# Kernel tuning notes

Measured on AMD Instinct MI355X. Metric: run time of the kernel, lower is better.

Reference implementation:

```python
import jax, jax.numpy as jnp
import numpy as np

N_NODES = 50000
D_IN = 128
D_OUT = 128
N_EDGES = 800000


def setup_inputs() -> dict:
    key = jax.random.key(0)
    k1, k2, k3, k4 = jax.random.split(key, 4)
    x = jax.random.normal(k1, (N_NODES, D_IN), dtype=jnp.float32)
    # nn.Linear(input_size, output_size, bias=False): weight is [out, in], y = x @ W.T.
    # We store W1 as [in, out] so y = x @ W1 (same math, transposed storage).
    W1 = jax.random.normal(k2, (D_IN, D_OUT), dtype=jnp.float32) * (1.0 / np.sqrt(D_IN))
    row = jax.random.randint(k3, (N_EDGES,), 0, N_NODES, dtype=jnp.int64)
    col = jax.random.randint(k4, (N_EDGES,), 0, N_NODES, dtype=jnp.int64)
    edge_index = jnp.stack([row, col], axis=0)  # [2, E]
    return {"x": x, "W1": W1, "edge_index": edge_index}


def reference(x, W1, edge_index):
    # Linear transform: [N, D_in] @ [D_in, D_out] -> [N, D_out]
    norm_m = x @ W1
    adj_row = edge_index[0]  # source nodes (gather)
    adj_col = edge_index[1]  # destination nodes (scatter)
    gathered = norm_m[adj_row]  # [E, D_out]
    pooled = jax.ops.segment_max(gathered, adj_col, num_segments=x.shape[0])
    # torch_scatter fills segments with no incoming edges with 0 (not -inf)
    deg = jax.ops.segment_sum(jnp.ones_like(adj_col, dtype=jnp.int32), adj_col,
                              num_segments=x.shape[0])
    pooled = jnp.where((deg > 0)[:, None], pooled, jnp.zeros_like(pooled))
    return jnp.concatenate((x, pooled), axis=1)  # [N, D_in + D_out]
```

## Files before the change

kernel.cpp:

```cpp
#include <hip/hip_runtime.h>


#define N_DIN 128
#define CAP 64
#define CURSTRIDE 16

typedef __attribute__((ext_vector_type(8))) short bf16x8;
typedef __attribute__((ext_vector_type(4))) float f32x4;

__device__ __forceinline__ short f32_bf16(float f) {
    unsigned u = __float_as_uint(f);
    return (short)((u + 0x7fffu + ((u >> 16) & 1u)) >> 16);
}

__global__ __launch_bounds__(256) void wconv(const float* __restrict__ W,
                                             short* __restrict__ Wt) {
    int i = blockIdx.x * 256 + threadIdx.x;
    int k = i >> 5, n0 = (i & 31) * 4;
    float4 v = *(const float4*)(W + k * 128 + n0);
    Wt[(n0 + 0) * 128 + k] = f32_bf16(v.x);
    Wt[(n0 + 1) * 128 + k] = f32_bf16(v.y);
    Wt[(n0 + 2) * 128 + k] = f32_bf16(v.z);
    Wt[(n0 + 3) * 128 + k] = f32_bf16(v.w);
}

__global__ __launch_bounds__(256) void scatter_direct(const int* __restrict__ row,
                                                      const int* __restrict__ col,
                                                      int* __restrict__ cur,
                                                      int* __restrict__ csrc, int E) {
    int e = blockIdx.x * 256 + threadIdx.x;
    if (e >= E) return;
    int dst = col[e];
    int pos = atomicAdd(&cur[dst * CURSTRIDE], 1);
    if (pos < CAP) csrc[dst * CAP + pos] = row[e];
}

__global__ __launch_bounds__(256) void gemm_mfma(const float* __restrict__ X,
                                                 const short* __restrict__ Wt,
                                                 short* __restrict__ Yb,
                                                 float* __restrict__ out, int N) {
    __shared__ short c_lds[4][32][128];
    const int tid = threadIdx.x;
    const int w = tid >> 6, l = tid & 63;
    const int lr = l & 15, lg = l >> 4;
    const int R0 = blockIdx.x * 128 + w * 32;

    bf16x8 af[2][4];
#pragma unroll
    for (int rt = 0; rt < 2; ++rt) {
        int gr = R0 + rt * 16 + lr;
        int grc = gr < N ? gr : N - 1;
#pragma unroll
        for (int t = 0; t < 4; ++t) {
            int kc = t * 32 + lg * 8;
            float4 v0 = *(const float4*)(X + (size_t)grc * 128 + kc);
            float4 v1 = *(const float4*)(X + (size_t)grc * 128 + kc + 4);
            if (gr < N) {
                *(float4*)(out + (size_t)gr * 256 + kc)     = v0;
                *(float4*)(out + (size_t)gr * 256 + kc + 4) = v1;
            }
            bf16x8 a;
            a[0] = f32_bf16(v0.x); a[1] = f32_bf16(v0.y);
            a[2] = f32_bf16(v0.z); a[3] = f32_bf16(v0.w);
            a[4] = f32_bf16(v1.x); a[5] = f32_bf16(v1.y);
            a[6] = f32_bf16(v1.z); a[7] = f32_bf16(v1.w);
            af[rt][t] = a;
        }
    }
#pragma unroll
    for (int ct = 0; ct < 8; ++ct) {
        f32x4 c0 = {0.f, 0.f, 0.f, 0.f}, c1 = {0.f, 0.f, 0.f, 0.f};
        const short* bp = Wt + (ct * 16 + lr) * 128;
#pragma unroll
        for (int t = 0; t < 4; ++t) {
            bf16x8 b = *(const bf16x8*)(bp + t * 32 + lg * 8);
            c0 = __builtin_amdgcn_mfma_f32_16x16x32_bf16(af[0][t], b, c0, 0, 0, 0);
            c1 = __builtin_amdgcn_mfma_f32_16x16x32_bf16(af[1][t], b, c1, 0, 0, 0);
        }
#pragma unroll
        for (int i = 0; i < 4; ++i) {
            c_lds[w][lg * 4 + i][ct * 16 + lr]      = f32_bf16(c0[i]);
            c_lds[w][16 + lg * 4 + i][ct * 16 + lr] = f32_bf16(c1[i]);
        }
    }
#pragma unroll
    for (int it = 0; it < 8; ++it) {
        int cid = it * 64 + l;
        int r2 = cid >> 4, c2 = cid & 15;
        int gr = R0 + r2;
        if (gr < N) {
            bf16x8 vv = *(const bf16x8*)(&c_lds[w][r2][c2 * 8]);
            *(bf16x8*)(Yb + (size_t)gr * 128 + c2 * 8) = vv;
        }
    }
}

__global__ __launch_bounds__(256) void pool_bf16(const unsigned* __restrict__ nmb,
                                                 const int* __restrict__ cur,
                                                 const int* __restrict__ csrc,
                                                 float* __restrict__ out, int N) {
    int node = blockIdx.x * 4 + (threadIdx.x >> 6);
    if (node >= N) return;
    int lane = threadIdx.x & 63;
    int deg = cur[node * CURSTRIDE];
    if (deg > CAP) deg = CAP;
    const int* lst = csrc + node * CAP;
    float2 acc = make_float2(-INFINITY, -INFINITY);
    int j = 0;
    for (; j + 4 <= deg; j += 4) {
        int s0 = lst[j], s1 = lst[j + 1], s2 = lst[j + 2], s3 = lst[j + 3];
        unsigned v0 = nmb[s0 * 64 + lane];
        unsigned v1 = nmb[s1 * 64 + lane];
        unsigned v2 = nmb[s2 * 64 + lane];
        unsigned v3 = nmb[s3 * 64 + lane];
        acc.x = fmaxf(acc.x, fmaxf(fmaxf(__uint_as_float(v0 << 16), __uint_as_float(v1 << 16)),
                                   fmaxf(__uint_as_float(v2 << 16), __uint_as_float(v3 << 16))));
        acc.y = fmaxf(acc.y, fmaxf(fmaxf(__uint_as_float(v0 & 0xffff0000u), __uint_as_float(v1 & 0xffff0000u)),
                                   fmaxf(__uint_as_float(v2 & 0xffff0000u), __uint_as_float(v3 & 0xffff0000u))));
    }
    for (; j < deg; ++j) {
        unsigned v0 = nmb[lst[j] * 64 + lane];
        acc.x = fmaxf(acc.x, __uint_as_float(v0 << 16));
        acc.y = fmaxf(acc.y, __uint_as_float(v0 & 0xffff0000u));
    }
    if (deg == 0) acc = make_float2(0.f, 0.f);
    *(float2*)(out + (size_t)node * 256 + N_DIN + lane * 2) = acc;
}

extern "C" void kernel_launch(void* const* d_in, const int* in_sizes, int n_in,
                              void* d_out, int out_size, void* d_ws, size_t ws_size,
                              hipStream_t stream) {
    const float* x  = (const float*)d_in[0];
    const float* W1 = (const float*)d_in[1];
    const int* ei   = (const int*)d_in[2];
    const int N = in_sizes[0] / N_DIN;
    const int E = in_sizes[2] / 2;
    const int* row = ei;
    const int* col = ei + E;
    float* out = (float*)d_out;

    short* norm_mb = (short*)d_ws;
    short* Wt = norm_mb + (size_t)N * N_DIN;
    int* cur  = (int*)(Wt + 128 * 128);
    int* csrc = cur + (size_t)N * CURSTRIDE;

    hipMemsetAsync(cur, 0, (size_t)N * CURSTRIDE * sizeof(int), stream);
    wconv<<<16, 256, 0, stream>>>(W1, Wt);
    scatter_direct<<<(E + 255) / 256, 256, 0, stream>>>(row, col, cur, csrc, E);
    gemm_mfma<<<(N + 127) / 128, 256, 0, stream>>>(x, Wt, norm_mb, out, N);
    pool_bf16<<<(N + 3) / 4, 256, 0, stream>>>((const unsigned*)norm_mb, cur, csrc, out, N);
}
```

Measured before the change: 187.2 us.

## Fuse edge scatter into GEMM launch and compact CSR index storage

Merges the edge-bucketing scatter kernel into the MFMA GEMM kernel as extra blocks so both run concurrently in one launch. Removes the 16-int padding on per-node counters, shrinking the memset and the counter footprint. Stores neighbor source indices as 16-bit values, halving index traffic in the scatter and pool phases. This relies on the node count fitting in 16 bits. The unpadded counters may add some atomic contention within cache lines.

```diff
diff --git a/kernel.cpp b/kernel.cpp
--- a/kernel.cpp
+++ b/kernel.cpp
@@ -3,7 +3,6 @@
 
 #define N_DIN 128
 #define CAP 64
-#define CURSTRIDE 16
 
 typedef __attribute__((ext_vector_type(8))) short bf16x8;
 typedef __attribute__((ext_vector_type(4))) float f32x4;
@@ -24,26 +23,26 @@
     Wt[(n0 + 3) * 128 + k] = f32_bf16(v.w);
 }
 
-__global__ __launch_bounds__(256) void scatter_direct(const int* __restrict__ row,
-                                                      const int* __restrict__ col,
-                                                      int* __restrict__ cur,
-                                                      int* __restrict__ csrc, int E) {
-    int e = blockIdx.x * 256 + threadIdx.x;
-    if (e >= E) return;
-    int dst = col[e];
-    int pos = atomicAdd(&cur[dst * CURSTRIDE], 1);
-    if (pos < CAP) csrc[dst * CAP + pos] = row[e];
-}
-
-__global__ __launch_bounds__(256) void gemm_mfma(const float* __restrict__ X,
-                                                 const short* __restrict__ Wt,
-                                                 short* __restrict__ Yb,
-                                                 float* __restrict__ out, int N) {
+__global__ __launch_bounds__(256) void fused_gemm_scatter(
+        const float* __restrict__ X, const short* __restrict__ Wt,
+        short* __restrict__ Yb, float* __restrict__ out, int N, int gblocks,
+        const int* __restrict__ row, const int* __restrict__ col,
+        int* __restrict__ cur, unsigned short* __restrict__ csrc, int E) {
+    if ((int)blockIdx.x >= gblocks) {
+        int e = ((int)blockIdx.x - gblocks) * 256 + (int)threadIdx.x;
+        if (e < E) {
+            int dst = col[e];
+            int pos = atomicAdd(&cur[dst], 1);
+            if (pos < CAP)
+                csrc[dst * CAP + pos] = (unsigned short)row[e];
+        }
+        return;
+    }
     __shared__ short c_lds[4][32][128];
     const int tid = threadIdx.x;
     const int w = tid >> 6, l = tid & 63;
     const int lr = l & 15, lg = l >> 4;
-    const int R0 = blockIdx.x * 128 + w * 32;
+    const int R0 = (int)blockIdx.x * 128 + w * 32;
 
     bf16x8 af[2][4];
 #pragma unroll
@@ -97,14 +96,14 @@
 
 __global__ __launch_bounds__(256) void pool_bf16(const unsigned* __restrict__ nmb,
                                                  const int* __restrict__ cur,
-                                                 const int* __restrict__ csrc,
+                                                 const unsigned short* __restrict__ csrc,
                                                  float* __restrict__ out, int N) {
     int node = blockIdx.x * 4 + (threadIdx.x >> 6);
     if (node >= N) return;
     int lane = threadIdx.x & 63;
-    int deg = cur[node * CURSTRIDE];
+    int deg = cur[node];
     if (deg > CAP) deg = CAP;
-    const int* lst = csrc + node * CAP;
+    const unsigned short* lst = csrc + node * CAP;
     float2 acc = make_float2(-INFINITY, -INFINITY);
     int j = 0;
     for (; j + 4 <= deg; j += 4) {
@@ -142,11 +141,14 @@
     short* norm_mb = (short*)d_ws;
     short* Wt = norm_mb + (size_t)N * N_DIN;
     int* cur  = (int*)(Wt + 128 * 128);
-    int* csrc = cur + (size_t)N * CURSTRIDE;
+    unsigned short* csrc = (unsigned short*)(cur + N);
 
-    hipMemsetAsync(cur, 0, (size_t)N * CURSTRIDE * sizeof(int), stream);
+    const int gblocks = (N + 127) / 128;
+    const int sblocks = (E + 255) / 256;
+
+    hipMemsetAsync(cur, 0, (size_t)N * sizeof(int), stream);
     wconv<<<16, 256, 0, stream>>>(W1, Wt);
-    scatter_direct<<<(E + 255) / 256, 256, 0, stream>>>(row, col, cur, csrc, E);
-    gemm_mfma<<<(N + 127) / 128, 256, 0, stream>>>(x, Wt, norm_mb, out, N);
+    fused_gemm_scatter<<<gblocks + sblocks, 256, 0, stream>>>(
+        x, Wt, norm_mb, out, N, gblocks, row, col, cur, csrc, E);
     pool_bf16<<<(N + 3) / 4, 256, 0, stream>>>((const unsigned*)norm_mb, cur, csrc, out, N);
 }
```

Measured after the change: 168.6 us. 9.9% less time.
